# Performance work log

Measured on AMD Instinct MI355X. Metric: run time of the kernel, lower is better.

## Reference

```python
import jax, jax.numpy as jnp
import numpy as np

A, E, O = 8, 4096, 256          # agents, envs-per-agent, obs dim
H1, H2, H3 = 1024, 1024, 512     # idims
S = 4                            # number of shared (SEPS) networks


def setup_inputs() -> dict:
    key = jax.random.key(0)
    ks = jax.random.split(key, 8)
    f32 = jnp.float32
    return {
        "x": jax.random.normal(ks[0], (A, E, O), f32),
        "W1": jax.random.normal(ks[1], (S, O, H1), f32) * (1.0 / np.sqrt(O)),
        "b1": jnp.zeros((S, H1), f32),
        "W2": jax.random.normal(ks[2], (S, H1, H2), f32) * (np.sqrt(2.0) / np.sqrt(H1)),
        "b2": jnp.zeros((S, H2), f32),
        "W3": jax.random.normal(ks[3], (S, H2, H3), f32) * (np.sqrt(2.0) / np.sqrt(H2)),
        "b3": jnp.zeros((S, H3), f32),
        "seps_idx": jax.random.randint(ks[4], (A,), 0, S, dtype=jnp.int64),
    }


def reference(x, W1, b1, W2, b2, W3, b3, seps_idx):
    # x: [A, E, O]. Each of the S nets is applied (as in the original Python
    # loop) to the full stacked input, then the per-agent output is gathered
    # by seps_idx. MLP: Linear -> ReLU -> Linear -> ReLU -> Linear.
    def mlp(w1, bb1, w2, bb2, w3, bb3):
        h = jax.nn.relu(jnp.einsum('aeo,oh->aeh', x, w1) + bb1)
        h = jax.nn.relu(jnp.einsum('aeh,hg->aeg', h, w2) + bb2)
        return jnp.einsum('aeg,gk->aek', h, w3) + bb3

    out = jax.vmap(mlp)(W1, b1, W2, b2, W3, b3)           # [S, A, E, H3]
    sel = out[seps_idx, jnp.arange(A)]                    # [A, E, H3]
    return sel
```

## Files before the change

### kernel.cpp

```cpp
#include <hip/hip_runtime.h>
#include <hip/hip_bf16.h>


typedef unsigned short u16;
typedef __bf16 bf16x8 __attribute__((ext_vector_type(8)));
typedef float floatx4 __attribute__((ext_vector_type(4)));
typedef unsigned short ushort8 __attribute__((ext_vector_type(8)));

__device__ __forceinline__ u16 f2bf(float f) {
    union { float f; unsigned int u; } v; v.f = f;
    unsigned int u = v.u;
    return (u16)((u + 0x7FFFu + ((u >> 16) & 1u)) >> 16);
}

__device__ __forceinline__ void load16(const void* g, void* l) {
    __builtin_amdgcn_global_load_lds(
        (const __attribute__((address_space(1))) void*)(unsigned long long)g,
        (__attribute__((address_space(3))) void*)(unsigned int)(unsigned long long)l,
        16, 0, 0);
}

__global__ __launch_bounds__(256) void prep(
    const float* __restrict__ x, u16* __restrict__ xb,
    const float* __restrict__ W1, u16* __restrict__ w1t,
    const float* __restrict__ W2, u16* __restrict__ w2t,
    const float* __restrict__ W3, u16* __restrict__ w3t) {
    __shared__ float tile[32][33];
    int b = blockIdx.x;
    const int tid = threadIdx.x;
    if (b < 8192) {
        int i = (b * 256 + tid) * 4;
        float4 v = *(const float4*)(x + i);
        ushort4 o;
        o.x = f2bf(v.x); o.y = f2bf(v.y); o.z = f2bf(v.z); o.w = f2bf(v.w);
        *(ushort4*)(xb + i) = o;
        return;
    }
    b -= 8192;
    const float* src; u16* dst; int K, N, n0, k0, s;
    if (b < 1024) {
        s = b >> 8; int r = b & 255;
        K = 256; N = 1024; n0 = (r & 31) * 32; k0 = (r >> 5) * 32;
        src = W1; dst = w1t;
    } else if (b < 5120) {
        b -= 1024; s = b >> 10; int r = b & 1023;
        K = 1024; N = 1024; n0 = (r & 31) * 32; k0 = (r >> 5) * 32;
        src = W2; dst = w2t;
    } else {
        b -= 5120; s = b >> 9; int r = b & 511;
        K = 1024; N = 512; n0 = (r & 15) * 32; k0 = (r >> 4) * 32;
        src = W3; dst = w3t;
    }
    src += (size_t)s * K * N;
    dst += (size_t)s * N * K;
    const int tx = tid & 31, ty = tid >> 5;
#pragma unroll
    for (int j = 0; j < 32; j += 8)
        tile[ty + j][tx] = src[(size_t)(k0 + ty + j) * N + (n0 + tx)];
    __syncthreads();
#pragma unroll
    for (int j = 0; j < 32; j += 8)
        dst[(size_t)(n0 + ty + j) * K + (k0 + tx)] = f2bf(tile[tx][ty + j]);
}

template <int K, int N, bool RELU, bool OUT_BF16>
__global__ __launch_bounds__(256) void gemm_mlp(
    const u16* __restrict__ Amat, const u16* __restrict__ Wt,
    const float* __restrict__ bias, const int* __restrict__ seps,
    void* __restrict__ outp) {
    constexpr int BM = 128, BN = 128, BK = 64;
    constexpr int NIT = K / BK;
    constexpr int NNB = N / 128;
    constexpr int LNB = (NNB == 8) ? 3 : 2;
    constexpr int EW = 132;
    __shared__ u16 lds[4 * 8192];
    float* eps = (float*)lds;

    const int tid = threadIdx.x;
    const int wave = tid >> 6, lane = tid & 63;
    const int wm = wave >> 1, wn = wave & 1;
    const int quad = lane >> 4, l16 = lane & 15;

    const int bidx = blockIdx.x;
    const int t = bidx >> 3;
    const int mb = (t >> LNB) * 8 + (bidx & 7);
    const int nb = t & (NNB - 1);
    const int m0 = mb * BM;
    const int n0 = nb * BN;

    const int s = seps[m0 >> 12];
    const u16* Ab = Amat + (size_t)m0 * K;
    const u16* Bb = Wt + ((size_t)s * N + n0) * K;

    const int srow = lane >> 3;
    const int sk = ((lane & 7) ^ (lane >> 3)) * 8;

    floatx4 acc[4][4];
#pragma unroll
    for (int i = 0; i < 4; ++i)
#pragma unroll
        for (int j = 0; j < 4; ++j) acc[i][j] = (floatx4){0.f, 0.f, 0.f, 0.f};

#pragma unroll
    for (int j = 0; j < 4; ++j) {
        const int c = wave * 4 + j;
        const int row = c * 8 + srow;
        load16(Ab + (size_t)row * K + sk, &lds[c * 512]);
        load16(Bb + (size_t)row * K + sk, &lds[8192 + c * 512]);
    }

    for (int it = 0; it < NIT; ++it) {
        __syncthreads();
        if (it + 1 < NIT) {
            const int k0 = (it + 1) * BK;
            u16* dstb = &lds[((it + 1) & 1) * 16384];
#pragma unroll
            for (int j = 0; j < 4; ++j) {
                const int c = wave * 4 + j;
                const int row = c * 8 + srow;
                load16(Ab + (size_t)row * K + k0 + sk, dstb + c * 512);
                load16(Bb + (size_t)row * K + k0 + sk, dstb + 8192 + c * 512);
            }
        }
        const u16* smA = &lds[(it & 1) * 16384];
        const u16* smB = smA + 8192;
#pragma unroll
        for (int h = 0; h < 2; ++h) {
            const int slot = ((h * 4 + quad) ^ (l16 & 7)) * 8;
            bf16x8 af[4], bfv[4];
#pragma unroll
            for (int t2 = 0; t2 < 4; ++t2) {
                af[t2]  = *(const bf16x8*)&smA[(wm * 64 + t2 * 16 + l16) * 64 + slot];
                bfv[t2] = *(const bf16x8*)&smB[(wn * 64 + t2 * 16 + l16) * 64 + slot];
            }
#pragma unroll
            for (int mt = 0; mt < 4; ++mt)
#pragma unroll
                for (int nt = 0; nt < 4; ++nt)
                    acc[mt][nt] = __builtin_amdgcn_mfma_f32_16x16x32_bf16(
                        af[mt], bfv[nt], acc[mt][nt], 0, 0, 0);
        }
    }
    __syncthreads();

    float bv[4];
#pragma unroll
    for (int nt = 0; nt < 4; ++nt)
        bv[nt] = bias[s * N + n0 + wn * 64 + nt * 16 + l16];

    const int rr = tid >> 4;
    const int cg = tid & 15;

#pragma unroll
    for (int mt = 0; mt < 4; ++mt) {
#pragma unroll
        for (int nt = 0; nt < 4; ++nt) {
#pragma unroll
            for (int r2 = 0; r2 < 4; ++r2) {
                float v = acc[mt][nt][r2] + bv[nt];
                if (RELU) v = fmaxf(v, 0.0f);
                eps[(wm * 16 + quad * 4 + r2) * EW + wn * 64 + nt * 16 + l16] = v;
            }
        }
        __syncthreads();
#pragma unroll
        for (int p = 0; p < 2; ++p) {
            const int lrow = p * 16 + rr;
            const int grow = m0 + ((lrow < 16) ? (mt * 16 + lrow)
                                               : (64 + mt * 16 + (lrow - 16)));
            const float* src = eps + lrow * EW + cg * 8;
            float4 v0 = *(const float4*)(src);
            float4 v1 = *(const float4*)(src + 4);
            if (OUT_BF16) {
                ushort8 o;
                o[0] = f2bf(v0.x); o[1] = f2bf(v0.y); o[2] = f2bf(v0.z); o[3] = f2bf(v0.w);
                o[4] = f2bf(v1.x); o[5] = f2bf(v1.y); o[6] = f2bf(v1.z); o[7] = f2bf(v1.w);
                *(ushort8*)((u16*)outp + (size_t)grow * N + n0 + cg * 8) = o;
            } else {
                float* dst = (float*)outp + (size_t)grow * N + n0 + cg * 8;
                *(float4*)dst = v0;
                *(float4*)(dst + 4) = v1;
            }
        }
        __syncthreads();
    }
}

extern "C" void kernel_launch(void* const* d_in, const int* in_sizes, int n_in,
                              void* d_out, int out_size, void* d_ws, size_t ws_size,
                              hipStream_t stream) {
    const float* x  = (const float*)d_in[0];
    const float* W1 = (const float*)d_in[1];
    const float* b1 = (const float*)d_in[2];
    const float* W2 = (const float*)d_in[3];
    const float* b2 = (const float*)d_in[4];
    const float* W3 = (const float*)d_in[5];
    const float* b3 = (const float*)d_in[6];
    const int* seps = (const int*)d_in[7];

    char* ws = (char*)d_ws;
    u16* w1t = (u16*)(ws);
    u16* w2t = (u16*)(ws + (2ull << 20));
    u16* w3t = (u16*)(ws + (10ull << 20));
    u16* xb  = (u16*)(ws + (14ull << 20));
    u16* h1  = (u16*)(ws + (30ull << 20));
    u16* h2  = (u16*)(ws + (94ull << 20));

    prep<<<15360, 256, 0, stream>>>(x, xb, W1, w1t, W2, w2t, W3, w3t);

    gemm_mlp<256, 1024, true, true><<<2048, 256, 0, stream>>>(xb, w1t, b1, seps, h1);
    gemm_mlp<1024, 1024, true, true><<<2048, 256, 0, stream>>>(h1, w2t, b2, seps, h2);
    gemm_mlp<1024, 512, false, false><<<1024, 256, 0, stream>>>(h2, w3t, b3, seps, d_out);
}
```

Measured before the change: 277.1 us.

## Use 256x256 tiles with 4-stage LDS pipeline and 8-wave blocks

Each GEMM block grows from 128x128 with 4 waves to 256x256 with 8 waves. The K step drops to 32, and a 4-deep ring of 128KB of dynamic LDS is fed by direct global-to-LDS loads. Explicit vmcnt waits, barriers, sched_barrier and setprio split each K step into two MFMA phases that overlap the next stage's loads. The aim is more data reuse per tile and better hiding of memory latency. The cost is heavy LDS use, which limits occupancy to one block per CU, and fewer blocks overall (256 for the last layer), which may leave CUs idle at the tail.

```diff
diff --git a/kernel.cpp b/kernel.cpp
--- a/kernel.cpp
+++ b/kernel.cpp
@@ -64,122 +64,131 @@
 }
 
 template <int K, int N, bool RELU, bool OUT_BF16>
-__global__ __launch_bounds__(256) void gemm_mlp(
+__global__ __launch_bounds__(512, 2) void gemm_mlp(
     const u16* __restrict__ Amat, const u16* __restrict__ Wt,
     const float* __restrict__ bias, const int* __restrict__ seps,
     void* __restrict__ outp) {
-    constexpr int BM = 128, BN = 128, BK = 64;
-    constexpr int NIT = K / BK;
-    constexpr int NNB = N / 128;
-    constexpr int LNB = (NNB == 8) ? 3 : 2;
-    constexpr int EW = 132;
-    __shared__ u16 lds[4 * 8192];
-    float* eps = (float*)lds;
+    constexpr int BM = 256, BK = 32;
+    constexpr int NT = K / BK;
+    constexpr int NHT = 4 * NT;
+    constexpr int NNB = N / 256;
+    constexpr int LNB = (NNB == 4) ? 2 : 1;
+    extern __shared__ u16 lds[];
 
     const int tid = threadIdx.x;
     const int wave = tid >> 6, lane = tid & 63;
-    const int wm = wave >> 1, wn = wave & 1;
+    const int wm = wave >> 2, wn = wave & 3;
     const int quad = lane >> 4, l16 = lane & 15;
 
     const int bidx = blockIdx.x;
     const int t = bidx >> 3;
     const int mb = (t >> LNB) * 8 + (bidx & 7);
     const int nb = t & (NNB - 1);
-    const int m0 = mb * BM;
-    const int n0 = nb * BN;
+    const int m0 = mb * BM, n0 = nb * 256;
 
     const int s = seps[m0 >> 12];
     const u16* Ab = Amat + (size_t)m0 * K;
     const u16* Bb = Wt + ((size_t)s * N + n0) * K;
 
-    const int srow = lane >> 3;
-    const int sk = ((lane & 7) ^ (lane >> 3)) * 8;
-
-    floatx4 acc[4][4];
-#pragma unroll
-    for (int i = 0; i < 4; ++i)
+    const int soff = ((wave << 4) + (lane >> 2)) * K
+                   + (((lane & 3) ^ ((lane >> 2) & 3)) << 3);
+    u16* const ldsw = &lds[wave << 9];
+
+    auto STAGE = [&](int sh) {
+        if (sh < NHT) {
+            const int tl = sh >> 2, ht = sh & 3;
+            const u16* g = (ht & 2) ? Bb : Ab;
+            if (ht & 1) g += 128 * K;
+            load16(g + tl * BK + soff, ldsw + ((tl & 3) << 14) + (ht << 12));
+        }
+    };
+
+    floatx4 acc[8][4];
+#pragma unroll
+    for (int i = 0; i < 8; ++i)
 #pragma unroll
         for (int j = 0; j < 4; ++j) acc[i][j] = (floatx4){0.f, 0.f, 0.f, 0.f};
 
 #pragma unroll
-    for (int j = 0; j < 4; ++j) {
-        const int c = wave * 4 + j;
-        const int row = c * 8 + srow;
-        load16(Ab + (size_t)row * K + sk, &lds[c * 512]);
-        load16(Bb + (size_t)row * K + sk, &lds[8192 + c * 512]);
-    }
-
-    for (int it = 0; it < NIT; ++it) {
+    for (int sh = 0; sh < 8; ++sh) STAGE(sh);
+    asm volatile("s_waitcnt vmcnt(4)" ::: "memory");
+    __builtin_amdgcn_s_barrier();
+
+    const int aslot = (quad ^ (l16 & 3)) << 3;
+    const int arow = (wm << 7) + l16;
+    const int brow = (wn << 6) + l16;
+
+#pragma unroll 1
+    for (int T = 0; T < NT; ++T) {
+        const u16* buf = &lds[(T & 3) << 14];
+        const int sb = (T + 2) << 2;
+        bf16x8 bfr[4];
+#pragma unroll
+        for (int q = 0; q < 2; ++q) {
+            bf16x8 af[4];
+#pragma unroll
+            for (int i = 0; i < 4; ++i)
+                af[i] = *(const bf16x8*)&buf[((arow + (q << 6) + (i << 4)) << 5) + aslot];
+            if (q == 0) {
+#pragma unroll
+                for (int nf = 0; nf < 4; ++nf)
+                    bfr[nf] = *(const bf16x8*)&buf[8192 + ((brow + (nf << 4)) << 5) + aslot];
+            }
+            STAGE(sb + (q << 1));
+            STAGE(sb + (q << 1) + 1);
+            if (q == 1) {
+                if (T < NT - 2) asm volatile("s_waitcnt vmcnt(4)" ::: "memory");
+                else            asm volatile("s_waitcnt vmcnt(0)" ::: "memory");
+            }
+            __builtin_amdgcn_s_barrier();
+            asm volatile("s_waitcnt lgkmcnt(0)" ::: "memory");
+            __builtin_amdgcn_sched_barrier(0);
+            __builtin_amdgcn_s_setprio(1);
+#pragma unroll
+            for (int i = 0; i < 4; ++i)
+#pragma unroll
+                for (int nf = 0; nf < 4; ++nf)
+                    acc[(q << 2) + i][nf] = __builtin_amdgcn_mfma_f32_16x16x32_bf16(
+                        af[i], bfr[nf], acc[(q << 2) + i][nf], 0, 0, 0);
+            __builtin_amdgcn_s_setprio(0);
+            __builtin_amdgcn_sched_barrier(0);
+            __builtin_amdgcn_s_barrier();
+        }
+    }
+    __syncthreads();
+
+    float* eps = (float*)lds;
+    constexpr int EW = 268;
+    float bv[4];
+#pragma unroll
+    for (int nf = 0; nf < 4; ++nf)
+        bv[nf] = bias[s * N + n0 + (wn << 6) + (nf << 4) + l16];
+
+    const int rL = tid & 63;
+    const int rw = tid >> 6;
+
+#pragma unroll
+    for (int mf = 0; mf < 8; ++mf) {
+#pragma unroll
+        for (int nf = 0; nf < 4; ++nf)
+#pragma unroll
+            for (int r = 0; r < 4; ++r) {
+                float v = acc[mf][nf][r] + bv[nf];
+                if (RELU) v = fmaxf(v, 0.0f);
+                eps[((wm << 4) + (quad << 2) + r) * EW + (wn << 6) + (nf << 4) + l16] = v;
+            }
         __syncthreads();
-        if (it + 1 < NIT) {
-            const int k0 = (it + 1) * BK;
-            u16* dstb = &lds[((it + 1) & 1) * 16384];
-#pragma unroll
-            for (int j = 0; j < 4; ++j) {
-                const int c = wave * 4 + j;
-                const int row = c * 8 + srow;
-                load16(Ab + (size_t)row * K + k0 + sk, dstb + c * 512);
-                load16(Bb + (size_t)row * K + k0 + sk, dstb + 8192 + c * 512);
-            }
-        }
-        const u16* smA = &lds[(it & 1) * 16384];
-        const u16* smB = smA + 8192;
-#pragma unroll
-        for (int h = 0; h < 2; ++h) {
-            const int slot = ((h * 4 + quad) ^ (l16 & 7)) * 8;
-            bf16x8 af[4], bfv[4];
-#pragma unroll
-            for (int t2 = 0; t2 < 4; ++t2) {
-                af[t2]  = *(const bf16x8*)&smA[(wm * 64 + t2 * 16 + l16) * 64 + slot];
-                bfv[t2] = *(const bf16x8*)&smB[(wn * 64 + t2 * 16 + l16) * 64 + slot];
-            }
-#pragma unroll
-            for (int mt = 0; mt < 4; ++mt)
-#pragma unroll
-                for (int nt = 0; nt < 4; ++nt)
-                    acc[mt][nt] = __builtin_amdgcn_mfma_f32_16x16x32_bf16(
-                        af[mt], bfv[nt], acc[mt][nt], 0, 0, 0);
-        }
-    }
-    __syncthreads();
-
-    float bv[4];
-#pragma unroll
-    for (int nt = 0; nt < 4; ++nt)
-        bv[nt] = bias[s * N + n0 + wn * 64 + nt * 16 + l16];
-
-    const int rr = tid >> 4;
-    const int cg = tid & 15;
-
-#pragma unroll
-    for (int mt = 0; mt < 4; ++mt) {
-#pragma unroll
-        for (int nt = 0; nt < 4; ++nt) {
-#pragma unroll
-            for (int r2 = 0; r2 < 4; ++r2) {
-                float v = acc[mt][nt][r2] + bv[nt];
-                if (RELU) v = fmaxf(v, 0.0f);
-                eps[(wm * 16 + quad * 4 + r2) * EW + wn * 64 + nt * 16 + l16] = v;
-            }
-        }
-        __syncthreads();
-#pragma unroll
-        for (int p = 0; p < 2; ++p) {
-            const int lrow = p * 16 + rr;
-            const int grow = m0 + ((lrow < 16) ? (mt * 16 + lrow)
-                                               : (64 + mt * 16 + (lrow - 16)));
-            const float* src = eps + lrow * EW + cg * 8;
-            float4 v0 = *(const float4*)(src);
-            float4 v1 = *(const float4*)(src + 4);
+#pragma unroll
+        for (int j = 0; j < 4; ++j) {
+            const int er = rw + (j << 3);
+            const int grow = m0 + ((er >> 4) << 7) + (mf << 4) + (er & 15);
+            const float4 v = *(const float4*)&eps[er * EW + (rL << 2)];
             if (OUT_BF16) {
-                ushort8 o;
-                o[0] = f2bf(v0.x); o[1] = f2bf(v0.y); o[2] = f2bf(v0.z); o[3] = f2bf(v0.w);
-                o[4] = f2bf(v1.x); o[5] = f2bf(v1.y); o[6] = f2bf(v1.z); o[7] = f2bf(v1.w);
-                *(ushort8*)((u16*)outp + (size_t)grow * N + n0 + cg * 8) = o;
+                ushort4 o;
+                o.x = f2bf(v.x); o.y = f2bf(v.y); o.z = f2bf(v.z); o.w = f2bf(v.w);
+                *(ushort4*)((u16*)outp + (size_t)grow * N + n0 + (rL << 2)) = o;
             } else {
-                float* dst = (float*)outp + (size_t)grow * N + n0 + cg * 8;
-                *(float4*)dst = v0;
-                *(float4*)(dst + 4) = v1;
+                *(float4*)((float*)outp + (size_t)grow * N + n0 + (rL << 2)) = v;
             }
         }
         __syncthreads();
@@ -206,9 +215,23 @@
     u16* h1  = (u16*)(ws + (30ull << 20));
     u16* h2  = (u16*)(ws + (94ull << 20));
 
+    static int attr_once = []() {
+        auto k1 = gemm_mlp<256, 1024, true, true>;
+        auto k2 = gemm_mlp<1024, 1024, true, true>;
+        auto k3 = gemm_mlp<1024, 512, false, false>;
+        hipFuncSetAttribute(reinterpret_cast<const void*>(k1),
+                            hipFuncAttributeMaxDynamicSharedMemorySize, 131072);
+        hipFuncSetAttribute(reinterpret_cast<const void*>(k2),
+                            hipFuncAttributeMaxDynamicSharedMemorySize, 131072);
+        hipFuncSetAttribute(reinterpret_cast<const void*>(k3),
+                            hipFuncAttributeMaxDynamicSharedMemorySize, 131072);
+        return 0;
+    }();
+    (void)attr_once;
+
     prep<<<15360, 256, 0, stream>>>(x, xb, W1, w1t, W2, w2t, W3, w3t);
 
-    gemm_mlp<256, 1024, true, true><<<2048, 256, 0, stream>>>(xb, w1t, b1, seps, h1);
-    gemm_mlp<1024, 1024, true, true><<<2048, 256, 0, stream>>>(h1, w2t, b2, seps, h2);
-    gemm_mlp<1024, 512, false, false><<<1024, 256, 0, stream>>>(h2, w3t, b3, seps, d_out);
-}
+    gemm_mlp<256, 1024, true, true><<<512, 512, 131072, stream>>>(xb, w1t, b1, seps, h1);
+    gemm_mlp<1024, 1024, true, true><<<512, 512, 131072, stream>>>(h1, w2t, b2, seps, h2);
+    gemm_mlp<1024, 512, false, false><<<256, 512, 131072, stream>>>(h2, w3t, b3, seps, d_out);
+}
```

Measured after the change: 278.0 us. Within noise of the previous version (+0.3%).
